# Optimization experiments

Measured on AMD Instinct MI355X. Metric: run time of the kernel, lower is better.

## Reference

```python
import jax, jax.numpy as jnp
import numpy as np

MS_KS = 9
C = 256
BN_EPS = 1e-5


def setup_inputs() -> dict:
    key = jax.random.key(0)
    k1, k2, k3 = jax.random.split(key, 3)
    p2_r = jax.random.normal(k1, (2, C, 64, 128), dtype=jnp.float32)
    conv_w = jax.random.normal(k2, (C, C, 1, MS_KS), dtype=jnp.float32) * 0.02
    conv1_w = jax.random.normal(k3, (1, C, 1, 1), dtype=jnp.float32) * 0.05
    bn_gamma = jnp.ones((1,), jnp.float32)
    bn_beta = jnp.zeros((1,), jnp.float32)
    return dict(p2_r=p2_r, conv_w=conv_w, conv1_w=conv1_w,
                bn_gamma=bn_gamma, bn_beta=bn_beta)


def _scnn_pass(x, M):
    # x: [b,c,h,w]. Each step applies conv(1,ms_ks) to a width-1 column with
    # zero padding ms_ks//2 -> only the center tap contributes, i.e. a 256x256
    # channel matmul per column, followed by relu and residual add.
    cols = jnp.moveaxis(x, 3, 0)  # [w,b,c,h]
    def step(carry, col):
        new = col + jax.nn.relu(jnp.einsum('oc,bch->boh', M, carry))
        return new, new
    _, outs = jax.lax.scan(step, cols[0], cols[1:])
    outs = jnp.concatenate([cols[:1], outs], axis=0)[::-1]  # mirrors out[::-1]
    return jnp.moveaxis(outs, 0, 3)


def _upsample_bilinear_ac(x, factor=4):
    # F.interpolate(mode='bilinear', align_corners=True)
    b, c, h, w = x.shape
    Ho, Wo = factor * h, factor * w
    ys = jnp.arange(Ho, dtype=x.dtype) * ((h - 1) / (Ho - 1))
    xs = jnp.arange(Wo, dtype=x.dtype) * ((w - 1) / (Wo - 1))
    y0 = jnp.floor(ys).astype(jnp.int32)
    y1 = jnp.minimum(y0 + 1, h - 1)
    wy = (ys - y0.astype(x.dtype))[None, None, :, None]
    rows = x[:, :, y0, :] * (1 - wy) + x[:, :, y1, :] * wy  # [b,c,Ho,w]
    x0 = jnp.floor(xs).astype(jnp.int32)
    x1 = jnp.minimum(x0 + 1, w - 1)
    wx = (xs - x0.astype(x.dtype))[None, None, None, :]
    return rows[:, :, :, x0] * (1 - wx) + rows[:, :, :, x1] * wx


def reference(p2_r, conv_w, conv1_w, bn_gamma, bn_beta):
    M = conv_w[:, :, 0, MS_KS // 2]  # center tap, [c_out, c_in]
    x = _scnn_pass(p2_r, M)                     # reverse=False
    x = _scnn_pass(x[:, :, :, ::-1], M)         # reverse=True (slices[::-1])
    x = _upsample_bilinear_ac(x, 4)             # [b,256,4h,4w]
    x = jnp.einsum('oc,bchw->bohw', conv1_w[:, :, 0, 0], x)  # 1x1 conv -> 1 ch
    # BatchNorm2d(1), training-mode batch statistics (biased variance)
    mean = jnp.mean(x, axis=(0, 2, 3), keepdims=True)
    var = jnp.mean((x - mean) ** 2, axis=(0, 2, 3), keepdims=True)
    x = (x - mean) * jax.lax.rsqrt(var + BN_EPS)
    x = x * bn_gamma[None, :, None, None] + bn_beta[None, :, None, None]
    return jax.nn.sigmoid(x)
```

## Files before the change

kernel.cpp:

```cpp
#include <hip/hip_runtime.h>


typedef _Float16 f16x8 __attribute__((ext_vector_type(8)));
typedef _Float16 f16x4 __attribute__((ext_vector_type(4)));
typedef float    f32x4 __attribute__((ext_vector_type(4)));

static __device__ __forceinline__ void sync_lds() {
  asm volatile("s_waitcnt lgkmcnt(0)" ::: "memory");
  __builtin_amdgcn_s_barrier();
  asm volatile("" ::: "memory");
}

static __device__ __forceinline__ float dpp_even(float v) {
  int t = __builtin_bit_cast(int, v);
  t = __builtin_amdgcn_update_dpp(t, t, 0xA0, 0xF, 0xF, false);
  return __builtin_bit_cast(float, t);
}

extern "C" __global__ void k_extract(const float* __restrict__ convw,
                                     _Float16* __restrict__ Md) {
  int q = blockIdx.x * 256 + threadIdx.x;
  float4 v = ((const float4*)convw)[q];
  float vv[4] = {v.x, v.y, v.z, v.w};
  int f = q * 4;
#pragma unroll
  for (int e = 0; e < 4; ++e) {
    int flat = f + e;
    if (flat % 9 == 4) Md[flat / 9] = (_Float16)vv[e];
  }
}

struct SM {
  _Float16 cy[2][256];
  _Float16 pad_[32];
  _Float16 zh[128 * 256];
};

extern "C" __global__ void __launch_bounds__(512, 2)
k_scan(const float* __restrict__ p2, const _Float16* __restrict__ Md,
       const float* __restrict__ conv1, float* __restrict__ sout,
       float* __restrict__ stats) {
  __shared__ SM sm;
  const int tid  = threadIdx.x;
  const int l    = tid & 63;
  const int r    = tid >> 6;
  const int col  = l & 15;
  const int quad = l >> 4;
  const int b    = blockIdx.x >> 6;
  const int h    = blockIdx.x & 63;

  if (blockIdx.x == 0 && tid == 0) { stats[0] = 0.f; stats[1] = 0.f; }

  const bool isY   = (col == 0);
  const bool isZ   = (col == 1);
  const bool zlane = (l & 1);

  const int m0 = (r * 2 + 0) * 16 + quad * 4;
  const int m1 = (r * 2 + 1) * 16 + quad * 4;

  f16x8 A0[8], A1[8];
#pragma unroll
  for (int ch = 0; ch < 8; ++ch) {
    A0[ch] = *(const f16x8*)(Md + ((r*2+0)*16 + col) * 256 + ch*32 + quad*8);
    A1[ch] = *(const f16x8*)(Md + ((r*2+1)*16 + col) * 256 + ch*32 + quad*8);
  }

  const float* pbase = p2 + (size_t)b * 2097152 + (size_t)h * 128;

  if (isY) {
    float c0a[4], c0b[4];
#pragma unroll
    for (int i = 0; i < 4; ++i) {
      c0a[i] = pbase[(size_t)(m0 + i) * 8192];
      c0b[i] = pbase[(size_t)(m1 + i) * 8192];
    }
    f16x4 pa, pb;
#pragma unroll
    for (int i = 0; i < 4; ++i) { pa[i] = (_Float16)c0a[i]; pb[i] = (_Float16)c0b[i]; }
    *(f16x4*)(sm.cy[0] + m0) = pa; *(f16x4*)(sm.cy[0] + m1) = pb;
    *(f16x4*)(sm.zh    + m0) = pa; *(f16x4*)(sm.zh    + m1) = pb;
  }

  float cca[4], ccb[4], cna[4], cnb[4];
  if (isY) {
#pragma unroll
    for (int i = 0; i < 4; ++i) {
      cca[i] = pbase[(size_t)(m0 + i) * 8192 + 1];
      ccb[i] = pbase[(size_t)(m1 + i) * 8192 + 1];
      cna[i] = pbase[(size_t)(m0 + i) * 8192 + 2];
      cnb[i] = pbase[(size_t)(m1 + i) * 8192 + 2];
    }
  }
  sync_lds();

  const _Float16* pY0 = sm.cy[0] + quad * 8;
  const _Float16* pY1 = sm.cy[1] + quad * 8;
  const _Float16* zrd = sm.zh + quad * 8;
  _Float16*       zwr = sm.zh + 256;

#define STEP(W, PY, WY, CA, CB)                                                \
  do {                                                                         \
    const _Float16* bsrc = zlane ? zrd : (PY);                                 \
    f16x8 B[8];                                                                \
    _Pragma("unroll")                                                          \
    for (int ch = 0; ch < 8; ++ch)                                             \
      B[ch] = *(const f16x8*)(bsrc + ch * 32);                                 \
    f32x4 a00 = {0.f,0.f,0.f,0.f}, a01 = {0.f,0.f,0.f,0.f};                    \
    f32x4 a10 = {0.f,0.f,0.f,0.f}, a11 = {0.f,0.f,0.f,0.f};                    \
    _Pragma("unroll")                                                          \
    for (int ch = 0; ch < 4; ++ch) {                                           \
      a00 = __builtin_amdgcn_mfma_f32_16x16x32_f16(A0[ch],   B[ch],   a00,0,0,0);\
      a10 = __builtin_amdgcn_mfma_f32_16x16x32_f16(A1[ch],   B[ch],   a10,0,0,0);\
      a01 = __builtin_amdgcn_mfma_f32_16x16x32_f16(A0[ch+4], B[ch+4], a01,0,0,0);\
      a11 = __builtin_amdgcn_mfma_f32_16x16x32_f16(A1[ch+4], B[ch+4], a11,0,0,0);\
    }                                                                          \
    f32x4 acc0 = a00 + a01, acc1 = a10 + a11;                                  \
    f32x4 yf0 = {}, yf1 = {};                                                  \
    if (isY) {                                                                 \
      f16x4 yh0, yh1;                                                          \
      _Pragma("unroll")                                                        \
      for (int i = 0; i < 4; ++i) {                                            \
        yf0[i] = (CA)[i] + fmaxf(acc0[i], 0.f);                                \
        yf1[i] = (CB)[i] + fmaxf(acc1[i], 0.f);                                \
        yh0[i] = (_Float16)yf0[i]; yh1[i] = (_Float16)yf1[i];                  \
      }                                                                        \
      *(f16x4*)((WY) + m0) = yh0;                                              \
      *(f16x4*)((WY) + m1) = yh1;                                              \
      if ((W) + 2 < 128) {                                                     \
        _Pragma("unroll")                                                      \
        for (int i = 0; i < 4; ++i) {                                          \
          (CA)[i] = pbase[(size_t)(m0 + i) * 8192 + (W) + 2];                  \
          (CB)[i] = pbase[(size_t)(m1 + i) * 8192 + (W) + 2];                  \
        }                                                                      \
      }                                                                        \
    }                                                                          \
    _Pragma("unroll")                                                          \
    for (int i = 0; i < 4; ++i) {                                              \
      yf0[i] = dpp_even(yf0[i]);                                               \
      yf1[i] = dpp_even(yf1[i]);                                               \
    }                                                                          \
    if (isZ) {                                                                 \
      f16x4 zh0, zh1;                                                          \
      _Pragma("unroll")                                                        \
      for (int i = 0; i < 4; ++i) {                                            \
        zh0[i] = (_Float16)(yf0[i] + fmaxf(acc0[i], 0.f));                     \
        zh1[i] = (_Float16)(yf1[i] + fmaxf(acc1[i], 0.f));                     \
      }                                                                        \
      *(f16x4*)(zwr + m0) = zh0;                                               \
      *(f16x4*)(zwr + m1) = zh1;                                               \
    }                                                                          \
    zrd += 256; zwr += 256;                                                    \
    sync_lds();                                                                \
  } while (0)

#pragma unroll 1
  for (int w = 1; w < 127; w += 2) {
    STEP(w,     pY0, sm.cy[1], cca, ccb);
    STEP(w + 1, pY1, sm.cy[0], cna, cnb);
  }
  STEP(127, pY0, sm.cy[1], cca, ccb);
#undef STEP

  {
    const int w    = tid >> 2;
    const int part = tid & 3;
    const _Float16* zr = sm.zh + w * 256 + part * 64;
    const float*    vr = conv1 + part * 64;
    float s = 0.f;
#pragma unroll
    for (int j = 0; j < 8; ++j) {
      f16x8 zv = *(const f16x8*)(zr + j * 8);
      float4 v0 = *(const float4*)(vr + j * 8);
      float4 v1 = *(const float4*)(vr + j * 8 + 4);
      s += v0.x * (float)zv[0] + v0.y * (float)zv[1]
         + v0.z * (float)zv[2] + v0.w * (float)zv[3]
         + v1.x * (float)zv[4] + v1.y * (float)zv[5]
         + v1.z * (float)zv[6] + v1.w * (float)zv[7];
    }
    s += __shfl_xor(s, 1, 64);
    s += __shfl_xor(s, 2, 64);
    if (part == 0) sout[(blockIdx.x << 7) + (127 - w)] = s;
  }
}

static __device__ __forceinline__ float bilin(const float* __restrict__ s,
                                              int idx) {
  int bb  = idx >> 17;
  int rem = idx & 131071;
  int ho  = rem >> 9;
  int wo  = rem & 511;
  const float SY = 63.0f / 255.0f, SX = 127.0f / 511.0f;
  float fy = (float)ho * SY;
  int y0 = (int)fy; int y1 = min(y0 + 1, 63); float wy = fy - (float)y0;
  float fx = (float)wo * SX;
  int x0 = (int)fx; int x1 = min(x0 + 1, 127); float wx = fx - (float)x0;
  const float* sb = s + bb * 8192;
  float cA = sb[y0 * 128 + x0] * (1.f - wy) + sb[y1 * 128 + x0] * wy;
  float cB = sb[y0 * 128 + x1] * (1.f - wy) + sb[y1 * 128 + x1] * wy;
  return cA * (1.f - wx) + cB * wx;
}

extern "C" __global__ void k_stats(const float* __restrict__ s,
                                   float* __restrict__ stats) {
  int tid  = threadIdx.x;
  int base = blockIdx.x * 1024 + tid;
  float sum = 0.f, ssq = 0.f;
#pragma unroll
  for (int i = 0; i < 4; ++i) {
    float u = bilin(s, base + i * 256);
    sum += u; ssq += u * u;
  }
#pragma unroll
  for (int off = 32; off > 0; off >>= 1) {
    sum += __shfl_xor(sum, off, 64);
    ssq += __shfl_xor(ssq, off, 64);
  }
  __shared__ float ls[4], lq[4];
  int wv = tid >> 6;
  if ((tid & 63) == 0) { ls[wv] = sum; lq[wv] = ssq; }
  __syncthreads();
  if (tid == 0) {
    atomicAdd(&stats[0], ls[0] + ls[1] + ls[2] + ls[3]);
    atomicAdd(&stats[1], lq[0] + lq[1] + lq[2] + lq[3]);
  }
}

extern "C" __global__ void k_norm(const float* __restrict__ s,
                                  const float* __restrict__ stats,
                                  const float* __restrict__ gamma,
                                  const float* __restrict__ beta,
                                  float* __restrict__ out) {
  int tid  = threadIdx.x;
  int base = blockIdx.x * 1024 + tid;
  const float invN = 1.f / 262144.f;
  float mean  = stats[0] * invN;
  float var   = stats[1] * invN - mean * mean;
  float scale = rsqrtf(var + 1e-5f) * gamma[0];
  float bias  = beta[0] - mean * scale;
#pragma unroll
  for (int i = 0; i < 4; ++i) {
    int idx = base + i * 256;
    float u = bilin(s, idx);
    float x = u * scale + bias;
    out[idx] = 1.f / (1.f + __expf(-x));
  }
}

extern "C" void kernel_launch(void* const* d_in, const int* in_sizes, int n_in,
                              void* d_out, int out_size, void* d_ws, size_t ws_size,
                              hipStream_t stream) {
  const float* p2    = (const float*)d_in[0];
  const float* convw = (const float*)d_in[1];
  const float* conv1 = (const float*)d_in[2];
  const float* gamma = (const float*)d_in[3];
  const float* beta  = (const float*)d_in[4];
  float* out = (float*)d_out;

  char* ws = (char*)d_ws;
  float*    s     = (float*)ws;
  float*    stats = (float*)(ws + 65536);
  _Float16* Md    = (_Float16*)(ws + 65792);

  hipLaunchKernelGGL(k_extract, dim3(576), dim3(256), 0, stream, convw, Md);
  hipLaunchKernelGGL(k_scan,    dim3(128), dim3(512), 0, stream, p2, Md, conv1, s, stats);
  hipLaunchKernelGGL(k_stats,   dim3(256), dim3(256), 0, stream, s, stats);
  hipLaunchKernelGGL(k_norm,    dim3(256), dim3(256), 0, stream, s, stats, gamma, beta, out);
}
```

Before: 178.9 us.

## Halve scan block to four waves, each computing four 16-row output tiles

The scan kernel now runs 256 threads (4 waves) per block instead of 512 (8 waves). Each wave owns four 16-row tiles of the 256x256 matrix instead of two, keeping 32 A fragments in registers and issuing 16 MFMAs per half-step. The goal is cheaper per-step barriers, with fewer waves to synchronize, at the cost of a longer serial MFMA chain per wave and higher register pressure. The final conv1 reduction is re-split so each output column uses 2 threads instead of 4.

```diff
diff --git a/kernel.cpp b/kernel.cpp
--- a/kernel.cpp
+++ b/kernel.cpp
@@ -36,7 +36,7 @@
   _Float16 zh[128 * 256];
 };
 
-extern "C" __global__ void __launch_bounds__(512, 2)
+extern "C" __global__ void __launch_bounds__(256, 1)
 k_scan(const float* __restrict__ p2, const _Float16* __restrict__ Md,
        const float* __restrict__ conv1, float* __restrict__ sout,
        float* __restrict__ stats) {
@@ -55,41 +55,40 @@
   const bool isZ   = (col == 1);
   const bool zlane = (l & 1);
 
-  const int m0 = (r * 2 + 0) * 16 + quad * 4;
-  const int m1 = (r * 2 + 1) * 16 + quad * 4;
-
-  f16x8 A0[8], A1[8];
-#pragma unroll
-  for (int ch = 0; ch < 8; ++ch) {
-    A0[ch] = *(const f16x8*)(Md + ((r*2+0)*16 + col) * 256 + ch*32 + quad*8);
-    A1[ch] = *(const f16x8*)(Md + ((r*2+1)*16 + col) * 256 + ch*32 + quad*8);
-  }
+  int mrow[4];
+#pragma unroll
+  for (int t = 0; t < 4; ++t) mrow[t] = (r * 4 + t) * 16 + quad * 4;
+
+  f16x8 A[4][8];
+#pragma unroll
+  for (int t = 0; t < 4; ++t)
+#pragma unroll
+    for (int ch = 0; ch < 8; ++ch)
+      A[t][ch] = *(const f16x8*)(Md + ((r*4+t)*16 + col) * 256 + ch*32 + quad*8);
 
   const float* pbase = p2 + (size_t)b * 2097152 + (size_t)h * 128;
 
   if (isY) {
-    float c0a[4], c0b[4];
-#pragma unroll
-    for (int i = 0; i < 4; ++i) {
-      c0a[i] = pbase[(size_t)(m0 + i) * 8192];
-      c0b[i] = pbase[(size_t)(m1 + i) * 8192];
+#pragma unroll
+    for (int t = 0; t < 4; ++t) {
+      f16x4 p;
+#pragma unroll
+      for (int i = 0; i < 4; ++i)
+        p[i] = (_Float16)pbase[(size_t)(mrow[t] + i) * 8192];
+      *(f16x4*)(sm.cy[0] + mrow[t]) = p;
+      *(f16x4*)(sm.zh    + mrow[t]) = p;
     }
-    f16x4 pa, pb;
-#pragma unroll
-    for (int i = 0; i < 4; ++i) { pa[i] = (_Float16)c0a[i]; pb[i] = (_Float16)c0b[i]; }
-    *(f16x4*)(sm.cy[0] + m0) = pa; *(f16x4*)(sm.cy[0] + m1) = pb;
-    *(f16x4*)(sm.zh    + m0) = pa; *(f16x4*)(sm.zh    + m1) = pb;
-  }
-
-  float cca[4], ccb[4], cna[4], cnb[4];
+  }
+
+  float cc[4][4], cn[4][4];
   if (isY) {
 #pragma unroll
-    for (int i = 0; i < 4; ++i) {
-      cca[i] = pbase[(size_t)(m0 + i) * 8192 + 1];
-      ccb[i] = pbase[(size_t)(m1 + i) * 8192 + 1];
-      cna[i] = pbase[(size_t)(m0 + i) * 8192 + 2];
-      cnb[i] = pbase[(size_t)(m1 + i) * 8192 + 2];
-    }
+    for (int t = 0; t < 4; ++t)
+#pragma unroll
+      for (int i = 0; i < 4; ++i) {
+        cc[t][i] = pbase[(size_t)(mrow[t] + i) * 8192 + 1];
+        cn[t][i] = pbase[(size_t)(mrow[t] + i) * 8192 + 2];
+      }
   }
   sync_lds();
 
@@ -98,56 +97,64 @@
   const _Float16* zrd = sm.zh + quad * 8;
   _Float16*       zwr = sm.zh + 256;
 
-#define STEP(W, PY, WY, CA, CB)                                                \
+#define STEP(W, PY, WY, C)                                                     \
   do {                                                                         \
     const _Float16* bsrc = zlane ? zrd : (PY);                                 \
     f16x8 B[8];                                                                \
     _Pragma("unroll")                                                          \
     for (int ch = 0; ch < 8; ++ch)                                             \
       B[ch] = *(const f16x8*)(bsrc + ch * 32);                                 \
-    f32x4 a00 = {0.f,0.f,0.f,0.f}, a01 = {0.f,0.f,0.f,0.f};                    \
-    f32x4 a10 = {0.f,0.f,0.f,0.f}, a11 = {0.f,0.f,0.f,0.f};                    \
+    f32x4 a0[4], a1[4];                                                        \
+    _Pragma("unroll")                                                          \
+    for (int t = 0; t < 4; ++t) {                                              \
+      a0[t] = (f32x4){0.f, 0.f, 0.f, 0.f};                                     \
+      a1[t] = (f32x4){0.f, 0.f, 0.f, 0.f};                                     \
+    }                                                                          \
     _Pragma("unroll")                                                          \
     for (int ch = 0; ch < 4; ++ch) {                                           \
-      a00 = __builtin_amdgcn_mfma_f32_16x16x32_f16(A0[ch],   B[ch],   a00,0,0,0);\
-      a10 = __builtin_amdgcn_mfma_f32_16x16x32_f16(A1[ch],   B[ch],   a10,0,0,0);\
-      a01 = __builtin_amdgcn_mfma_f32_16x16x32_f16(A0[ch+4], B[ch+4], a01,0,0,0);\
-      a11 = __builtin_amdgcn_mfma_f32_16x16x32_f16(A1[ch+4], B[ch+4], a11,0,0,0);\
-    }                                                                          \
-    f32x4 acc0 = a00 + a01, acc1 = a10 + a11;                                  \
-    f32x4 yf0 = {}, yf1 = {};                                                  \
+      _Pragma("unroll")                                                        \
+      for (int t = 0; t < 4; ++t) {                                            \
+        a0[t] = __builtin_amdgcn_mfma_f32_16x16x32_f16(A[t][ch],   B[ch],   a0[t],0,0,0); \
+        a1[t] = __builtin_amdgcn_mfma_f32_16x16x32_f16(A[t][ch+4], B[ch+4], a1[t],0,0,0); \
+      }                                                                        \
+    }                                                                          \
+    f32x4 acc[4];                                                              \
+    _Pragma("unroll")                                                          \
+    for (int t = 0; t < 4; ++t) acc[t] = a0[t] + a1[t];                        \
+    f32x4 yf[4] = {};                                                          \
     if (isY) {                                                                 \
-      f16x4 yh0, yh1;                                                          \
-      _Pragma("unroll")                                                        \
-      for (int i = 0; i < 4; ++i) {                                            \
-        yf0[i] = (CA)[i] + fmaxf(acc0[i], 0.f);                                \
-        yf1[i] = (CB)[i] + fmaxf(acc1[i], 0.f);                                \
-        yh0[i] = (_Float16)yf0[i]; yh1[i] = (_Float16)yf1[i];                  \
-      }                                                                        \
-      *(f16x4*)((WY) + m0) = yh0;                                              \
-      *(f16x4*)((WY) + m1) = yh1;                                              \
+      _Pragma("unroll")                                                        \
+      for (int t = 0; t < 4; ++t) {                                            \
+        f16x4 yh;                                                              \
+        _Pragma("unroll")                                                      \
+        for (int i = 0; i < 4; ++i) {                                          \
+          yf[t][i] = (C)[t][i] + fmaxf(acc[t][i], 0.f);                        \
+          yh[i] = (_Float16)yf[t][i];                                          \
+        }                                                                      \
+        *(f16x4*)((WY) + mrow[t]) = yh;                                        \
+      }                                                                        \
       if ((W) + 2 < 128) {                                                     \
         _Pragma("unroll")                                                      \
-        for (int i = 0; i < 4; ++i) {                                          \
-          (CA)[i] = pbase[(size_t)(m0 + i) * 8192 + (W) + 2];                  \
-          (CB)[i] = pbase[(size_t)(m1 + i) * 8192 + (W) + 2];                  \
-        }                                                                      \
-      }                                                                        \
-    }                                                                          \
-    _Pragma("unroll")                                                          \
-    for (int i = 0; i < 4; ++i) {                                              \
-      yf0[i] = dpp_even(yf0[i]);                                               \
-      yf1[i] = dpp_even(yf1[i]);                                               \
-    }                                                                          \
+        for (int t = 0; t < 4; ++t)                                            \
+          _Pragma("unroll")                                                    \
+          for (int i = 0; i < 4; ++i)                                          \
+            (C)[t][i] = pbase[(size_t)(mrow[t] + i) * 8192 + (W) + 2];         \
+      }                                                                        \
+    }                                                                          \
+    _Pragma("unroll")                                                          \
+    for (int t = 0; t < 4; ++t)                                                \
+      _Pragma("unroll")                                                        \
+      for (int i = 0; i < 4; ++i)                                              \
+        yf[t][i] = dpp_even(yf[t][i]);                                         \
     if (isZ) {                                                                 \
-      f16x4 zh0, zh1;                                                          \
-      _Pragma("unroll")                                                        \
-      for (int i = 0; i < 4; ++i) {                                            \
-        zh0[i] = (_Float16)(yf0[i] + fmaxf(acc0[i], 0.f));                     \
-        zh1[i] = (_Float16)(yf1[i] + fmaxf(acc1[i], 0.f));                     \
-      }                                                                        \
-      *(f16x4*)(zwr + m0) = zh0;                                               \
-      *(f16x4*)(zwr + m1) = zh1;                                               \
+      _Pragma("unroll")                                                        \
+      for (int t = 0; t < 4; ++t) {                                            \
+        f16x4 zo;                                                              \
+        _Pragma("unroll")                                                      \
+        for (int i = 0; i < 4; ++i)                                            \
+          zo[i] = (_Float16)(yf[t][i] + fmaxf(acc[t][i], 0.f));                \
+        *(f16x4*)(zwr + mrow[t]) = zo;                                         \
+      }                                                                        \
     }                                                                          \
     zrd += 256; zwr += 256;                                                    \
     sync_lds();                                                                \
@@ -155,20 +162,20 @@
 
 #pragma unroll 1
   for (int w = 1; w < 127; w += 2) {
-    STEP(w,     pY0, sm.cy[1], cca, ccb);
-    STEP(w + 1, pY1, sm.cy[0], cna, cnb);
-  }
-  STEP(127, pY0, sm.cy[1], cca, ccb);
+    STEP(w,     pY0, sm.cy[1], cc);
+    STEP(w + 1, pY1, sm.cy[0], cn);
+  }
+  STEP(127, pY0, sm.cy[1], cc);
 #undef STEP
 
   {
-    const int w    = tid >> 2;
-    const int part = tid & 3;
-    const _Float16* zr = sm.zh + w * 256 + part * 64;
-    const float*    vr = conv1 + part * 64;
+    const int w    = tid >> 1;
+    const int part = tid & 1;
+    const _Float16* zr = sm.zh + w * 256 + part * 128;
+    const float*    vr = conv1 + part * 128;
     float s = 0.f;
 #pragma unroll
-    for (int j = 0; j < 8; ++j) {
+    for (int j = 0; j < 16; ++j) {
       f16x8 zv = *(const f16x8*)(zr + j * 8);
       float4 v0 = *(const float4*)(vr + j * 8);
       float4 v1 = *(const float4*)(vr + j * 8 + 4);
@@ -178,7 +185,6 @@
          + v1.z * (float)zv[6] + v1.w * (float)zv[7];
     }
     s += __shfl_xor(s, 1, 64);
-    s += __shfl_xor(s, 2, 64);
     if (part == 0) sout[(blockIdx.x << 7) + (127 - w)] = s;
   }
 }
@@ -262,7 +268,7 @@
   _Float16* Md    = (_Float16*)(ws + 65792);
 
   hipLaunchKernelGGL(k_extract, dim3(576), dim3(256), 0, stream, convw, Md);
-  hipLaunchKernelGGL(k_scan,    dim3(128), dim3(512), 0, stream, p2, Md, conv1, s, stats);
+  hipLaunchKernelGGL(k_scan,    dim3(128), dim3(256), 0, stream, p2, Md, conv1, s, stats);
   hipLaunchKernelGGL(k_stats,   dim3(256), dim3(256), 0, stream, s, stats);
   hipLaunchKernelGGL(k_norm,    dim3(256), dim3(256), 0, stream, s, stats, gamma, beta, out);
 }
```

Measured after the change: 202.2 us. 1.13x slower.
